# Kernel tuning notes

Measured on AMD Instinct MI355X. Metric: run time of the kernel, lower is better.

The kernel has to match this reference:

```python
import jax, jax.numpy as jnp
import numpy as np

T = 2048      # total tokens (single prefill sequence)
HID = 2048    # hidden_size
H = 16        # num k-heads == num v-heads
DK = 128      # key head dim
DV = 128      # value head dim
K = 4         # causal conv kernel width
EPS = 1e-6


def setup_inputs() -> dict:
    key = jax.random.key(0)
    ks = jax.random.split(key, 10)
    n = lambda k, shape, sc: (jax.random.normal(k, shape, jnp.float32) * sc)
    return {
        "hidden_states": n(ks[0], (T, HID), 1.0),
        "Wq": n(ks[1], (HID, H * DK), 0.02),
        "Wk": n(ks[2], (HID, H * DK), 0.02),
        "Wv": n(ks[3], (HID, H * DV), 0.02),
        "Wb": n(ks[4], (HID, H), 0.02),
        "conv_wq": n(ks[5], (H * DK, K), 0.5),
        "conv_wk": n(ks[6], (H * DK, K), 0.5),
        "conv_wv": n(ks[7], (H * DV, K), 0.5),
        "o_norm_w": jnp.ones((DV,), jnp.float32),
        "Wo": n(ks[8], (HID, HID), 0.02),
    }


def _causal_conv_silu(x, w):
    # x: [T, D], w: [D, K] depthwise causal conv, then SiLU (matches causal_conv1d_fn)
    xp = jnp.pad(x, ((K - 1, 0), (0, 0)))
    y = sum(xp[j:j + T] * w[:, j] for j in range(K))
    return jax.nn.silu(y)


def _l2norm(x):
    return x * jax.lax.rsqrt(jnp.sum(x * x, axis=-1, keepdims=True) + EPS)


def reference(hidden_states, Wq, Wk, Wv, Wb, conv_wq, conv_wk, conv_wv, o_norm_w, Wo):
    # projections [T, H*D]
    q = _causal_conv_silu(hidden_states @ Wq, conv_wq).reshape(T, H, DK)
    k = _causal_conv_silu(hidden_states @ Wk, conv_wk).reshape(T, H, DK)
    v = _causal_conv_silu(hidden_states @ Wv, conv_wv).reshape(T, H, DV)
    beta = jax.nn.sigmoid(hidden_states @ Wb)  # [T, H]

    # qk l2-norm + scale (FLA chunk_delta_rule defaults)
    q = _l2norm(q) * (DK ** -0.5)
    k = _l2norm(k)

    # delta-rule recurrence: S <- S + beta * k (v - k^T S)
    def step(S, inp):
        q_t, k_t, v_t, b_t = inp            # [H,DK],[H,DK],[H,DV],[H]
        kS = jnp.einsum('hk,hkv->hv', k_t, S)
        delta = b_t[:, None] * (v_t - kS)   # [H, DV]
        S = S + jnp.einsum('hk,hv->hkv', k_t, delta)
        o_t = jnp.einsum('hk,hkv->hv', q_t, S)
        return S, o_t

    S0 = jnp.zeros((H, DK, DV), jnp.float32)
    _, o = jax.lax.scan(step, S0, (q, k, v, beta))  # o: [T, H, DV]

    # per-head RMSNorm on value head dim
    o = o * jax.lax.rsqrt(jnp.mean(o * o, axis=-1, keepdims=True) + EPS) * o_norm_w
    out = o.reshape(T, H * DV) @ Wo
    return out
```

## Files before the change

### kernel.cpp

```cpp
#include <hip/hip_runtime.h>

typedef unsigned short u16;
typedef __attribute__((ext_vector_type(4))) unsigned short u16x4;
typedef __attribute__((ext_vector_type(8))) unsigned short u16x8;
typedef __attribute__((ext_vector_type(8))) short short8;
typedef __attribute__((ext_vector_type(4))) float f32x4;

#define DEVI __device__ __forceinline__

DEVI u16 f2b(float f) {
  union { float f; unsigned u; } x; x.f = f;
  unsigned r = (x.u + 0x7fffu + ((x.u >> 16) & 1u)) >> 16;
  return (u16)r;
}
DEVI float b2f(u16 h) {
  union { unsigned u; float f; } x; x.u = ((unsigned)h) << 16;
  return x.f;
}
DEVI f32x4 mfma_bf16(short8 a, short8 b, f32x4 c) {
  return __builtin_amdgcn_mfma_f32_16x16x32_bf16(a, b, c, 0, 0, 0);
}
DEVI void gl2lds16(const u16* g, u16* l) {
  __builtin_amdgcn_global_load_lds((__attribute__((address_space(1))) void*)g,
                                   (__attribute__((address_space(3))) void*)l,
                                   16, 0, 0);
}
DEVI void barrier_lds() {
  asm volatile("s_waitcnt lgkmcnt(0)\n\ts_barrier" ::: "memory");
}

__global__ void k_cvt(const float* __restrict__ src, u16* __restrict__ dst, int n4,
                      const float* __restrict__ Wb, u16* __restrict__ WbT) {
  int b = blockIdx.x;
  if (b < 4096) {
    int i = b * 256 + threadIdx.x;
    if (i < n4) {
      float4 v = ((const float4*)src)[i];
      u16x4 r; r.x = f2b(v.x); r.y = f2b(v.y); r.z = f2b(v.z); r.w = f2b(v.w);
      ((u16x4*)dst)[i] = r;
    }
  } else {
    int j = (b - 4096) * 256 + threadIdx.x;
    int n = j >> 11, k = j & 2047;
    WbT[j] = f2b(Wb[k * 16 + n]);
  }
}

__global__ __launch_bounds__(256)
void k_transpose4(const float* __restrict__ s0, const float* __restrict__ s1,
                  const float* __restrict__ s2, const float* __restrict__ s3,
                  u16* __restrict__ d0, u16* __restrict__ d1,
                  u16* __restrict__ d2, u16* __restrict__ d3) {
  const int RC = 2048;
  const float* src = (blockIdx.z == 0) ? s0 : (blockIdx.z == 1) ? s1 : (blockIdx.z == 2) ? s2 : s3;
  u16* dst = (blockIdx.z == 0) ? d0 : (blockIdx.z == 1) ? d1 : (blockIdx.z == 2) ? d2 : d3;
  __shared__ u16 tile[64 * 66];
  int bx = blockIdx.x << 6, by = blockIdx.y << 6;
  int x = threadIdx.x & 63, g = threadIdx.x >> 6;
#pragma unroll
  for (int i = 0; i < 16; ++i) {
    int r = (i << 2) + g;
    tile[x * 66 + r] = f2b(src[(size_t)(by + r) * RC + bx + x]);
  }
  __syncthreads();
#pragma unroll
  for (int i = 0; i < 16; ++i) {
    int r = (i << 2) + g;
    dst[(size_t)(bx + r) * RC + by + x] = tile[r * 66 + x];
  }
}

__global__ __launch_bounds__(256, 4)
void k_gemm_bt(const u16* __restrict__ A, const u16* __restrict__ BT,
               float* __restrict__ Cf, u16* __restrict__ Cb,
               int M, int N, int K, int outbf) {
  __shared__ __align__(16) u16 As[4096];
  __shared__ __align__(16) u16 Bs[4096];
  const int tid = threadIdx.x, wave = tid >> 6, lane = tid & 63;
  const long bm = (long)blockIdx.y << 7, bn = (long)blockIdx.x << 7;
  const int r0 = (wave << 4) + (lane >> 2);
  const int kof = (((lane & 3) ^ ((lane >> 3) & 3)) << 3);
  const u16* gA = A + (bm + r0) * (long)K + kof;
  const u16* gB = BT + (bn + r0) * (long)K + kof;
  u16* lA = As + (wave << 9);
  u16* lB = Bs + (wave << 9);
  const long stepR = (long)64 * K;
  const int wr = (wave >> 1) << 6, wc = (wave & 1) << 6;
  const int fr = lane & 15, fq = (lane >> 4) << 3;
  const int fqs = fq ^ (((fr >> 1) & 3) << 3);
  f32x4 acc[4][4];
#pragma unroll
  for (int i = 0; i < 4; ++i)
#pragma unroll
    for (int j = 0; j < 4; ++j) acc[i][j] = (f32x4){0.f, 0.f, 0.f, 0.f};
  for (int k0 = 0; k0 < K; k0 += 32) {
    gl2lds16(gA + k0, lA);
    gl2lds16(gA + stepR + k0, lA + 2048);
    gl2lds16(gB + k0, lB);
    gl2lds16(gB + stepR + k0, lB + 2048);
    __syncthreads();
    short8 af[4], bfr[4];
#pragma unroll
    for (int t = 0; t < 4; ++t)
      af[t] = *(const short8*)&As[(wr + (t << 4) + fr) * 32 + fqs];
#pragma unroll
    for (int t = 0; t < 4; ++t)
      bfr[t] = *(const short8*)&Bs[(wc + (t << 4) + fr) * 32 + fqs];
#pragma unroll
    for (int i = 0; i < 4; ++i)
#pragma unroll
      for (int j = 0; j < 4; ++j)
        acc[i][j] = mfma_bf16(af[i], bfr[j], acc[i][j]);
    __syncthreads();
  }
  const int er = (lane >> 4) << 2, ec = lane & 15;
#pragma unroll
  for (int i = 0; i < 4; ++i)
#pragma unroll
    for (int j = 0; j < 4; ++j)
#pragma unroll
      for (int r = 0; r < 4; ++r) {
        long row = bm + wr + (i << 4) + er + r;
        long col = bn + wc + (j << 4) + ec;
        if (outbf) Cb[row * N + col] = f2b(acc[i][j][r]);
        else       Cf[row * N + col] = acc[i][j][r];
      }
}

__global__ __launch_bounds__(256, 4)
void k_gemm_wo(const u16* __restrict__ A, const u16* __restrict__ BT,
               float* __restrict__ Cf, int M, int N, int K) {
  __shared__ __align__(16) u16 As[2048];
  __shared__ __align__(16) u16 Bs[2048];
  const int tid = threadIdx.x, wave = tid >> 6, lane = tid & 63;
  const long bm = (long)blockIdx.y << 6, bn = (long)blockIdx.x << 6;
  const int r0 = (wave << 4) + (lane >> 2);
  const int kof = (((lane & 3) ^ ((lane >> 3) & 3)) << 3);
  const u16* gA = A + (bm + r0) * (long)K + kof;
  const u16* gB = BT + (bn + r0) * (long)K + kof;
  u16* lA = As + (wave << 9);
  u16* lB = Bs + (wave << 9);
  const int wr = (wave >> 1) << 5, wc = (wave & 1) << 5;
  const int fr = lane & 15, fq = (lane >> 4) << 3;
  const int fqs = fq ^ (((fr >> 1) & 3) << 3);
  f32x4 acc[2][2];
#pragma unroll
  for (int i = 0; i < 2; ++i)
#pragma unroll
    for (int j = 0; j < 2; ++j) acc[i][j] = (f32x4){0.f, 0.f, 0.f, 0.f};
  for (int k0 = 0; k0 < K; k0 += 32) {
    gl2lds16(gA + k0, lA);
    gl2lds16(gB + k0, lB);
    __syncthreads();
    short8 af[2], bfr[2];
#pragma unroll
    for (int t = 0; t < 2; ++t) {
      af[t]  = *(const short8*)&As[(wr + (t << 4) + fr) * 32 + fqs];
      bfr[t] = *(const short8*)&Bs[(wc + (t << 4) + fr) * 32 + fqs];
    }
#pragma unroll
    for (int i = 0; i < 2; ++i)
#pragma unroll
      for (int j = 0; j < 2; ++j)
        acc[i][j] = mfma_bf16(af[i], bfr[j], acc[i][j]);
    __syncthreads();
  }
  const int er = (lane >> 4) << 2, ec = lane & 15;
#pragma unroll
  for (int i = 0; i < 2; ++i)
#pragma unroll
    for (int j = 0; j < 2; ++j)
#pragma unroll
      for (int r = 0; r < 4; ++r) {
        long row = bm + wr + (i << 4) + er + r;
        long col = bn + wc + (j << 4) + ec;
        Cf[row * N + col] = acc[i][j][r];
      }
}

__global__ __launch_bounds__(256, 4)
void k_beta(const u16* __restrict__ Xb, const u16* __restrict__ WbT,
            float* __restrict__ beta) {
  __shared__ float part[4][256];
  int tid = threadIdx.x, w = tid >> 6, lane = tid & 63;
  int t0 = blockIdx.x << 4;
  int fr = lane & 15, fq = (lane >> 4) << 3;
  const u16* ap = Xb + (size_t)(t0 + fr) * 2048 + (w << 9) + fq;
  const u16* bp = WbT + (size_t)fr * 2048 + (w << 9) + fq;
  f32x4 acc = {0.f, 0.f, 0.f, 0.f};
#pragma unroll
  for (int ks = 0; ks < 16; ++ks)
    acc = mfma_bf16(*(const short8*)(ap + (ks << 5)), *(const short8*)(bp + (ks << 5)), acc);
  int er = (lane >> 4) << 2;
#pragma unroll
  for (int r = 0; r < 4; ++r) part[w][(er + r) * 16 + fr] = acc[r];
  __syncthreads();
  float s = part[0][tid] + part[1][tid] + part[2][tid] + part[3][tid];
  beta[(t0 << 4) + tid] = 1.f / (1.f + __expf(-s));
}

__global__ __launch_bounds__(256, 4)
void k_conv(const u16* __restrict__ qkv,
            const float* __restrict__ cwq, const float* __restrict__ cwk,
            const float* __restrict__ cwv,
            u16* __restrict__ qn, u16* __restrict__ kn, u16* __restrict__ vn) {
  __shared__ __align__(16) u16 xs[67 * 136];
  __shared__ float wf[128 * 4];
  int tt = blockIdx.x, s = blockIdx.y;
  int kind = s >> 4, h = s & 15;
  int t0 = tt << 6;
  int col = (kind << 11) + (h << 7);
  int tid = threadIdx.x;
  const float* cw = (kind == 0) ? cwq : ((kind == 1) ? cwk : cwv);
  if (tid < 128) *(float4*)&wf[tid << 2] = *(const float4*)(cw + (size_t)((h << 7) + tid) * 4);
  for (int i = tid; i < 1072; i += 256) {
    int prow = i >> 4, c8 = (i & 15) << 3;
    int g = t0 - 3 + prow;
    u16x8 v = {0, 0, 0, 0, 0, 0, 0, 0};
    if (g >= 0) v = *(const u16x8*)(qkv + (size_t)g * 6144 + col + c8);
    *(u16x8*)&xs[prow * 136 + c8] = v;
  }
  __syncthreads();
  int t = tid >> 2, dg = tid & 3;
  float y[32];
  float ss = 0.f;
#pragma unroll
  for (int e8 = 0; e8 < 4; ++e8) {
    int d0 = (dg << 5) + (e8 << 3);
    u16x8 a0 = *(const u16x8*)&xs[(t + 0) * 136 + d0];
    u16x8 a1 = *(const u16x8*)&xs[(t + 1) * 136 + d0];
    u16x8 a2 = *(const u16x8*)&xs[(t + 2) * 136 + d0];
    u16x8 a3 = *(const u16x8*)&xs[(t + 3) * 136 + d0];
#pragma unroll
    for (int e = 0; e < 8; ++e) {
      float4 w = *(const float4*)&wf[(d0 + e) << 2];
      float v = b2f(a0[e]) * w.x + b2f(a1[e]) * w.y + b2f(a2[e]) * w.z + b2f(a3[e]) * w.w;
      v = v / (1.f + __expf(-v));
      y[(e8 << 3) + e] = v;
      ss += v * v;
    }
  }
  float sc = 1.f;
  if (kind < 2) {
    ss += __shfl_xor(ss, 1);
    ss += __shfl_xor(ss, 2);
    sc = rsqrtf(ss + 1e-6f);
    if (kind == 0) sc *= 0.08838834764831843f;
  }
  u16* dst = (kind == 0) ? qn : ((kind == 1) ? kn : vn);
  u16* dp = dst + ((size_t)h << 18) + ((size_t)(t0 + t) << 7) + (dg << 5);
#pragma unroll
  for (int e8 = 0; e8 < 4; ++e8) {
    u16x8 p;
#pragma unroll
    for (int e = 0; e < 8; ++e) p[e] = f2b(y[(e8 << 3) + e] * sc);
    *(u16x8*)(dp + (e8 << 3)) = p;
  }
}

__global__ __launch_bounds__(256, 2)
void k_prep(const u16* __restrict__ qn, const u16* __restrict__ kn, const u16* __restrict__ vn,
            const float* __restrict__ beta,
            u16* __restrict__ Gg, u16* __restrict__ Wg,
            u16* __restrict__ KTg, u16* __restrict__ UTg) {
  __shared__ __align__(16) char sm[70912];
  u16*  Kc  = (u16*)sm;
  u16*  Qc  = (u16*)(sm + 17408);
  u16*  Vc  = (u16*)(sm + 34816);
  u16*  KTl = (u16*)(sm + 52224);
  float* AL = (float*)(sm + 52224);
  float* Bl = (float*)(sm + 70656);
  u16*  WR  = Qc;
  int h = blockIdx.x, c = blockIdx.y;
  int tid = threadIdx.x, wave = tid >> 6, lane = tid & 63;
  size_t ch = (size_t)(c * 16 + h);
  const u16* kb = kn + ((size_t)h << 18) + ((size_t)c << 13);
  const u16* qb = qn + ((size_t)h << 18) + ((size_t)c << 13);
  const u16* vb = vn + ((size_t)h << 18) + ((size_t)c << 13);
#pragma unroll
  for (int s = 0; s < 4; ++s) {
    int e = (tid + (s << 8)) << 3;
    int t = e >> 7, d = e & 127;
    *(u16x8*)&Kc[t * 136 + d] = *(const u16x8*)(kb + e);
    *(u16x8*)&Qc[t * 136 + d] = *(const u16x8*)(qb + e);
    *(u16x8*)&Vc[t * 136 + d] = *(const u16x8*)(vb + e);
  }
  if (tid < 64) Bl[tid] = beta[((c << 6) + tid) * 16 + h];
  __syncthreads();
  int fr = lane & 15, fq = (lane >> 4) << 3, q4 = (lane >> 4) << 2;
  int arow = (wave << 4) + fr;
  f32x4 kk[4], qk[4];
#pragma unroll
  for (int ct = 0; ct < 4; ++ct) { kk[ct] = (f32x4){0.f,0.f,0.f,0.f}; qk[ct] = (f32x4){0.f,0.f,0.f,0.f}; }
#pragma unroll
  for (int ks = 0; ks < 4; ++ks) {
    short8 aK = *(const short8*)&Kc[arow * 136 + (ks << 5) + fq];
    short8 aQ = *(const short8*)&Qc[arow * 136 + (ks << 5) + fq];
#pragma unroll
    for (int ct = 0; ct < 4; ++ct) {
      short8 bK = *(const short8*)&Kc[((ct << 4) + fr) * 136 + (ks << 5) + fq];
      kk[ct] = mfma_bf16(aK, bK, kk[ct]);
      qk[ct] = mfma_bf16(aQ, bK, qk[ct]);
    }
  }
#pragma unroll
  for (int ct = 0; ct < 4; ++ct)
#pragma unroll
    for (int r = 0; r < 4; ++r) {
      int i = (wave << 4) + q4 + r, j = (ct << 4) + fr;
      Gg[(ch << 12) + i * 64 + j] = f2b((j <= i) ? qk[ct][r] : 0.f);
    }
  {
    int d = tid & 127, tg = tid >> 7;
#pragma unroll
    for (int it = 0; it < 4; ++it) {
      int t0 = (tg + (it << 1)) << 3;
      u16x8 pk;
#pragma unroll
      for (int j = 0; j < 8; ++j) pk[j] = Kc[(t0 + j) * 136 + d];
      *(u16x8*)&KTl[d * 72 + t0] = pk;
    }
  }
  __syncthreads();
#pragma unroll
  for (int it = 0; it < 4; ++it) {
    int idx = tid + (it << 8);
    int row = idx >> 3, j8 = (idx & 7) << 3;
    *(u16x8*)(KTg + (ch << 13) + (row << 6) + j8) = *(const u16x8*)&KTl[row * 72 + j8];
  }
  __syncthreads();
  {
    float bi[4];
#pragma unroll
    for (int r = 0; r < 4; ++r) bi[r] = Bl[(wave << 4) + q4 + r];
#pragma unroll
    for (int ct = 0; ct < 4; ++ct)
#pragma unroll
      for (int r = 0; r < 4; ++r) {
        int i = (wave << 4) + q4 + r, j = (ct << 4) + fr;
        AL[i * 64 + j] = (j < i) ? bi[r] * kk[ct][r] : 0.f;
      }
  }
  __syncthreads();
  float X[64];
  {
    const u16* colp = (tid < 128) ? (Kc + tid) : (Vc + (tid - 128));
#pragma unroll
    for (int t = 0; t < 64; ++t) X[t] = Bl[t] * b2f(colp[t * 136]);
#pragma unroll
    for (int r = 1; r < 64; ++r) {
      float s = 0.f;
      const float* Ar = &AL[r * 64];
      int r4 = r & ~3;
#pragma unroll
      for (int l = 0; l < 64; l += 4)
        if (l + 4 <= r) {
          float4 a = *(const float4*)(Ar + l);
          s += a.x * X[l] + a.y * X[l + 1] + a.z * X[l + 2] + a.w * X[l + 3];
        }
#pragma unroll
      for (int l = 0; l < 4; ++l)
        if (r4 + l < r) s += Ar[r4 + l] * X[r4 + l];
      X[r] -= s;
    }
  }
  __syncthreads();
  if (tid < 128) {
#pragma unroll
    for (int t = 0; t < 64; ++t) WR[t * 136 + tid] = f2b(X[t]);
  } else {
    int v = tid - 128;
    u16* dstr = UTg + (ch << 13) + (v << 6);
#pragma unroll
    for (int j = 0; j < 8; ++j) {
      u16x8 p;
#pragma unroll
      for (int e = 0; e < 8; ++e) p[e] = f2b(X[(j << 3) + e]);
      *(u16x8*)(dstr + (j << 3)) = p;
    }
  }
  __syncthreads();
#pragma unroll
  for (int it = 0; it < 4; ++it) {
    int idx = tid + (it << 8);
    int row = idx >> 4, j8 = (idx & 15) << 3;
    *(u16x8*)(Wg + (ch << 13) + (row << 7) + j8) = *(const u16x8*)&WR[row * 136 + j8];
  }
}

struct Frags { short8 q[4], w[4], g[2], k[4]; u16x4 u; };

DEVI void load_frags(Frags& f, const u16* qh, const u16* Wg, const u16* Gg,
                     const u16* KTg, const u16* UTg, int c, int h,
                     int trow, int fr, int fq, int q4, int w, int vbase) {
  const u16* qb = qh + ((size_t)((c << 6) + trow + fr) << 7) + fq;
#pragma unroll
  for (int ks = 0; ks < 4; ++ks) f.q[ks] = *(const short8*)(qb + (ks << 5));
  size_t ch = (size_t)(c * 16 + h);
  const u16* wb = Wg + (ch << 13) + ((size_t)(trow + fr) << 7) + fq;
#pragma unroll
  for (int ks = 0; ks < 4; ++ks) f.w[ks] = *(const short8*)(wb + (ks << 5));
  const u16* gb = Gg + (ch << 12) + ((size_t)(trow + fr) << 6) + fq;
#pragma unroll
  for (int ks = 0; ks < 2; ++ks) f.g[ks] = *(const short8*)(gb + (ks << 5));
  const u16* kbp = KTg + (ch << 13) + ((size_t)(w << 5) << 6) + fq;
#pragma unroll
  for (int dt = 0; dt < 2; ++dt)
#pragma unroll
    for (int ks = 0; ks < 2; ++ks)
      f.k[(dt << 1) | ks] = *(const short8*)(kbp + ((size_t)((dt << 4) + fr) << 6) + (ks << 5));
  f.u = *(const u16x4*)(UTg + (ch << 13) + ((size_t)(vbase + fr) << 6) + trow + q4);
}

DEVI void chunk_body(int c, Frags& f, u16* ST, u16* DT, u16* oh,
                     int trow, int fr, int fq, int q4, int w, int vbase,
                     f32x4& S0, f32x4& S1) {
#pragma unroll
  for (int r = 0; r < 4; ++r) {
    ST[(q4 + r) * 136 + (w << 5) + fr] = f2b(S0[r]);
    ST[(q4 + r) * 136 + (w << 5) + 16 + fr] = f2b(S1[r]);
  }
  barrier_lds();
  short8 sf[4];
#pragma unroll
  for (int ks = 0; ks < 4; ++ks) sf[ks] = *(const short8*)&ST[fr * 136 + (ks << 5) + fq];
  f32x4 racc = {0.f,0.f,0.f,0.f}, oacc = {0.f,0.f,0.f,0.f};
#pragma unroll
  for (int ks = 0; ks < 4; ++ks) {
    racc = mfma_bf16(f.w[ks], sf[ks], racc);
    oacc = mfma_bf16(f.q[ks], sf[ks], oacc);
  }
#pragma unroll
  for (int r = 0; r < 4; ++r)
    DT[fr * 72 + trow + q4 + r] = f2b(b2f(f.u[r]) - racc[r]);
  barrier_lds();
  short8 df[2];
#pragma unroll
  for (int ks = 0; ks < 2; ++ks) df[ks] = *(const short8*)&DT[fr * 72 + (ks << 5) + fq];
#pragma unroll
  for (int ks = 0; ks < 2; ++ks) {
    oacc = mfma_bf16(f.g[ks], df[ks], oacc);
    S0 = mfma_bf16(df[ks], f.k[ks], S0);
    S1 = mfma_bf16(df[ks], f.k[2 | ks], S1);
  }
#pragma unroll
  for (int r = 0; r < 4; ++r)
    oh[(size_t)((c << 6) + trow + q4 + r) * 128 + vbase + fr] = f2b(oacc[r]);
}

__global__ __launch_bounds__(256, 1)
void k_delta(const u16* __restrict__ qn, const u16* __restrict__ Wg,
             const u16* __restrict__ Gg, const u16* __restrict__ KTg,
             const u16* __restrict__ UTg, u16* __restrict__ o) {
  __shared__ __align__(16) u16 ST[16 * 136];
  __shared__ __align__(16) u16 DT[16 * 72];
  int bx = blockIdx.x;
  int h = bx & 15, vbase = (bx >> 4) << 4;
  int tid = threadIdx.x, w = tid >> 6, lane = tid & 63;
  int fr = lane & 15, fq = (lane >> 4) << 3, q4 = (lane >> 4) << 2;
  int trow = w << 4;
  const u16* qh = qn + ((size_t)h << 18);
  u16* oh = o + ((size_t)h << 18);
  f32x4 S0 = {0.f,0.f,0.f,0.f}, S1 = {0.f,0.f,0.f,0.f};
  Frags fa, fb;
  load_frags(fa, qh, Wg, Gg, KTg, UTg, 0, h, trow, fr, fq, q4, w, vbase);
  for (int c = 0; c < 32; c += 2) {
    int c1 = c + 1, c2 = (c + 2 < 32) ? c + 2 : 31;
    load_frags(fb, qh, Wg, Gg, KTg, UTg, c1, h, trow, fr, fq, q4, w, vbase);
    chunk_body(c, fa, ST, DT, oh, trow, fr, fq, q4, w, vbase, S0, S1);
    load_frags(fa, qh, Wg, Gg, KTg, UTg, c2, h, trow, fr, fq, q4, w, vbase);
    chunk_body(c1, fb, ST, DT, oh, trow, fr, fq, q4, w, vbase, S0, S1);
  }
}

__global__ __launch_bounds__(256, 4)
void k_onorm(const u16* __restrict__ o, const float* __restrict__ onw,
             u16* __restrict__ onb) {
  __shared__ float wl[128];
  int tt = blockIdx.x, h = blockIdx.y, tid = threadIdx.x;
  if (tid < 128) wl[tid] = onw[tid];
  __syncthreads();
  int t = tid >> 2, dg = tid & 3;
  const u16* src = o + ((size_t)h << 18) + ((size_t)((tt << 6) + t) << 7) + (dg << 5);
  u16x8 a[4];
  float ss = 0.f;
#pragma unroll
  for (int e8 = 0; e8 < 4; ++e8) {
    a[e8] = *(const u16x8*)(src + (e8 << 3));
#pragma unroll
    for (int e = 0; e < 8; ++e) { float x = b2f(a[e8][e]); ss += x * x; }
  }
  ss += __shfl_xor(ss, 1);
  ss += __shfl_xor(ss, 2);
  float inv = rsqrtf(ss * (1.f / 128.f) + 1e-6f);
  u16* dp = onb + ((size_t)((tt << 6) + t) << 11) + (h << 7) + (dg << 5);
#pragma unroll
  for (int e8 = 0; e8 < 4; ++e8) {
    u16x8 p;
#pragma unroll
    for (int e = 0; e < 8; ++e)
      p[e] = f2b(b2f(a[e8][e]) * inv * wl[(dg << 5) + (e8 << 3) + e]);
    *(u16x8*)(dp + (e8 << 3)) = p;
  }
}

extern "C" void kernel_launch(void* const* d_in, const int* in_sizes, int n_in,
                              void* d_out, int out_size, void* d_ws, size_t ws_size,
                              hipStream_t stream) {
  (void)in_sizes; (void)n_in; (void)out_size; (void)ws_size;
  const float* hs  = (const float*)d_in[0];
  const float* Wq  = (const float*)d_in[1];
  const float* Wk  = (const float*)d_in[2];
  const float* Wv  = (const float*)d_in[3];
  const float* Wb  = (const float*)d_in[4];
  const float* cwq = (const float*)d_in[5];
  const float* cwk = (const float*)d_in[6];
  const float* cwv = (const float*)d_in[7];
  const float* onw = (const float*)d_in[8];
  const float* Wo  = (const float*)d_in[9];
  float* out = (float*)d_out;
  char* ws = (char*)d_ws;
  const size_t MB = 1ull << 20;
  u16*  Xb   = (u16*)(ws);
  u16*  WT   = (u16*)(ws + 8  * MB);
  u16*  WoT  = (u16*)(ws + 32 * MB);
  u16*  QKV  = (u16*)(ws + 40 * MB);
  u16*  Wg   = (u16*)(ws + 40 * MB);
  u16*  KTg  = (u16*)(ws + 48 * MB);
  u16*  UTg  = (u16*)(ws + 56 * MB);
  u16*  qn_  = (u16*)(ws + 64 * MB);
  u16*  kn_  = (u16*)(ws + 72 * MB);
  u16*  vn_  = (u16*)(ws + 80 * MB);
  float* beta= (float*)(ws + 88 * MB);
  u16*  WbT  = (u16*)(ws + 88 * MB + 512 * 1024);
  u16*  Gm   = (u16*)(ws + 89 * MB);
  u16*  o_   = (u16*)(ws + 93 * MB);
  u16*  onb  = (u16*)(ws + 109 * MB);

  k_cvt<<<4224, 256, 0, stream>>>(hs, Xb, 2048 * 2048 / 4, Wb, WbT);
  k_transpose4<<<dim3(32, 32, 4), 256, 0, stream>>>(
      Wq, Wk, Wv, Wo, WT, WT + 2048 * 2048, WT + 2 * 2048 * 2048, WoT);
  k_gemm_bt<<<dim3(48, 16), 256, 0, stream>>>(Xb, WT, nullptr, QKV, 2048, 6144, 2048, 1);
  k_beta<<<128, 256, 0, stream>>>(Xb, WbT, beta);
  k_conv<<<dim3(32, 48), 256, 0, stream>>>(QKV, cwq, cwk, cwv, qn_, kn_, vn_);
  k_prep<<<dim3(16, 32), 256, 0, stream>>>(qn_, kn_, vn_, beta, Gm, Wg, KTg, UTg);
  k_delta<<<128, 256, 0, stream>>>(qn_, Wg, Gm, KTg, UTg, o_);
  k_onorm<<<dim3(32, 16), 256, 0, stream>>>(o_, onw, onb);
  k_gemm_wo<<<dim3(32, 32), 256, 0, stream>>>(onb, WoT, out, 2048, 2048, 2048);
}
```

Baseline: 345.4 us.

## Replace QKV GEMM with 256x256 tiled, double-buffered 8-wave pipelined kernel

Replaces the 128x128 single-buffered QKV projection GEMM with a 256x256-tile, 512-thread kernel that uses a 128 KB double-buffered LDS pipeline. Global-to-LDS loads for the next K-tile are issued in quarter-tile stages between MFMA phases, using explicit barriers, waitcnt and setprio. The intent is to raise data reuse per block and hide load latency behind tensor-core work. In exchange the grid shrinks to 192 blocks, which may underfill the CUs, and the hand-scheduled waits and swizzles add correctness risk.

```diff
diff --git a/kernel.cpp b/kernel.cpp
--- a/kernel.cpp
+++ b/kernel.cpp
@@ -70,61 +70,170 @@
   }
 }
 
-__global__ __launch_bounds__(256, 4)
-void k_gemm_bt(const u16* __restrict__ A, const u16* __restrict__ BT,
-               float* __restrict__ Cf, u16* __restrict__ Cb,
-               int M, int N, int K, int outbf) {
-  __shared__ __align__(16) u16 As[4096];
-  __shared__ __align__(16) u16 Bs[4096];
+
+struct StageCtx { size_t go[2]; int lo[2]; };
+
+DEVI void stage_half(const u16* g, const StageCtx& sc, u16* l) {
+  gl2lds16(g + sc.go[0], l + sc.lo[0]);
+  gl2lds16(g + sc.go[1], l + sc.lo[1]);
+}
+
+template <int MODE>
+DEVI void ktile8(const u16* gA0, const u16* gA1, const u16* gB0, const u16* gB1,
+                 const StageCtx& sc, u16* lds, int u,
+                 const int (&aoff)[4][2], const int (&boff)[2][2],
+                 f32x4 (&acc)[8][4]) {
+  const int sl = (u & 1) << 13, sl1 = ((u + 1) & 1) << 13;
+  const u16* hA0 = lds + sl;
+  const u16* hA1 = lds + 16384 + sl;
+  const u16* hB0 = lds + 32768 + sl;
+  const u16* hB1 = lds + 49152 + sl;
+  const size_t uo1 = (size_t)(u + 1) << 6, uo2 = (size_t)(u + 2) << 6;
+  short8 a[4][2], b0[2][2], b1[2][2];
+#pragma unroll
+  for (int m = 0; m < 4; ++m) {
+    a[m][0] = *(const short8*)(hA0 + aoff[m][0]);
+    a[m][1] = *(const short8*)(hA0 + aoff[m][1]);
+  }
+#pragma unroll
+  for (int n = 0; n < 2; ++n) {
+    b0[n][0] = *(const short8*)(hB0 + boff[n][0]);
+    b0[n][1] = *(const short8*)(hB0 + boff[n][1]);
+  }
+  if constexpr (MODE <= 1) stage_half(gA1 + uo1, sc, lds + 16384 + sl1);
+  __builtin_amdgcn_s_barrier();
+  asm volatile("s_waitcnt lgkmcnt(0)" ::: "memory");
+  __builtin_amdgcn_s_setprio(1);
+#pragma unroll
+  for (int m = 0; m < 4; ++m)
+#pragma unroll
+    for (int n = 0; n < 2; ++n) {
+      acc[m][n] = mfma_bf16(a[m][0], b0[n][0], acc[m][n]);
+      acc[m][n] = mfma_bf16(a[m][1], b0[n][1], acc[m][n]);
+    }
+  __builtin_amdgcn_s_setprio(0);
+  __builtin_amdgcn_s_barrier();
+#pragma unroll
+  for (int n = 0; n < 2; ++n) {
+    b1[n][0] = *(const short8*)(hB1 + boff[n][0]);
+    b1[n][1] = *(const short8*)(hB1 + boff[n][1]);
+  }
+  if constexpr (MODE == 0) stage_half(gA0 + uo2, sc, lds + sl);
+  __builtin_amdgcn_s_barrier();
+  asm volatile("s_waitcnt lgkmcnt(0)" ::: "memory");
+  __builtin_amdgcn_s_setprio(1);
+#pragma unroll
+  for (int m = 0; m < 4; ++m)
+#pragma unroll
+    for (int n = 0; n < 2; ++n) {
+      acc[m][2 + n] = mfma_bf16(a[m][0], b1[n][0], acc[m][2 + n]);
+      acc[m][2 + n] = mfma_bf16(a[m][1], b1[n][1], acc[m][2 + n]);
+    }
+  __builtin_amdgcn_s_setprio(0);
+  __builtin_amdgcn_s_barrier();
+#pragma unroll
+  for (int m = 0; m < 4; ++m) {
+    a[m][0] = *(const short8*)(hA1 + aoff[m][0]);
+    a[m][1] = *(const short8*)(hA1 + aoff[m][1]);
+  }
+  if constexpr (MODE == 0) stage_half(gB0 + uo2, sc, lds + 32768 + sl);
+  __builtin_amdgcn_s_barrier();
+  asm volatile("s_waitcnt lgkmcnt(0)" ::: "memory");
+  __builtin_amdgcn_s_setprio(1);
+#pragma unroll
+  for (int m = 0; m < 4; ++m)
+#pragma unroll
+    for (int n = 0; n < 2; ++n) {
+      acc[4 + m][n] = mfma_bf16(a[m][0], b0[n][0], acc[4 + m][n]);
+      acc[4 + m][n] = mfma_bf16(a[m][1], b0[n][1], acc[4 + m][n]);
+    }
+  __builtin_amdgcn_s_setprio(0);
+  __builtin_amdgcn_s_barrier();
+  if constexpr (MODE == 0) stage_half(gB1 + uo2, sc, lds + 49152 + sl);
+  __builtin_amdgcn_s_barrier();
+  __builtin_amdgcn_s_setprio(1);
+#pragma unroll
+  for (int m = 0; m < 4; ++m)
+#pragma unroll
+    for (int n = 0; n < 2; ++n) {
+      acc[4 + m][2 + n] = mfma_bf16(a[m][0], b1[n][0], acc[4 + m][2 + n]);
+      acc[4 + m][2 + n] = mfma_bf16(a[m][1], b1[n][1], acc[4 + m][2 + n]);
+    }
+  __builtin_amdgcn_s_setprio(0);
+  if constexpr (MODE == 0) asm volatile("s_waitcnt vmcnt(6)" ::: "memory");
+  if constexpr (MODE == 1) asm volatile("s_waitcnt vmcnt(0)" ::: "memory");
+  __builtin_amdgcn_s_barrier();
+}
+
+__global__ __launch_bounds__(512, 2)
+void k_gemm8p(const u16* __restrict__ A, const u16* __restrict__ BT,
+              u16* __restrict__ Cb, int N, int K) {
+  __shared__ __align__(16) u16 lds[65536];
   const int tid = threadIdx.x, wave = tid >> 6, lane = tid & 63;
-  const long bm = (long)blockIdx.y << 7, bn = (long)blockIdx.x << 7;
-  const int r0 = (wave << 4) + (lane >> 2);
-  const int kof = (((lane & 3) ^ ((lane >> 3) & 3)) << 3);
-  const u16* gA = A + (bm + r0) * (long)K + kof;
-  const u16* gB = BT + (bn + r0) * (long)K + kof;
-  u16* lA = As + (wave << 9);
-  u16* lB = Bs + (wave << 9);
-  const long stepR = (long)64 * K;
-  const int wr = (wave >> 1) << 6, wc = (wave & 1) << 6;
-  const int fr = lane & 15, fq = (lane >> 4) << 3;
-  const int fqs = fq ^ (((fr >> 1) & 3) << 3);
-  f32x4 acc[4][4];
-#pragma unroll
-  for (int i = 0; i < 4; ++i)
+  const int wm = wave >> 2, wn = wave & 3;
+  const int fr = lane & 15, fq = (lane >> 4) << 4;
+  const long bm = (long)blockIdx.y << 8, bn = (long)blockIdx.x << 8;
+  const int NT = K >> 6;
+  int aoff[4][2], boff[2][2];
+#pragma unroll
+  for (int m = 0; m < 4; ++m)
+#pragma unroll
+    for (int ks = 0; ks < 2; ++ks) {
+      int row = (wm << 6) + (m << 4) + fr;
+      int kb = (ks << 6) + fq;
+      aoff[m][ks] = (row << 6) + ((kb ^ ((fr & 7) << 4)) >> 1);
+    }
+#pragma unroll
+  for (int n = 0; n < 2; ++n)
+#pragma unroll
+    for (int ks = 0; ks < 2; ++ks) {
+      int row = (wn << 5) + (n << 4) + fr;
+      int kb = (ks << 6) + fq;
+      boff[n][ks] = (row << 6) + ((kb ^ ((fr & 7) << 4)) >> 1);
+    }
+  StageCtx sc;
+#pragma unroll
+  for (int s = 0; s < 2; ++s) {
+    int c = (s << 9) + tid, row = c >> 3;
+    int kbs = (((c & 7) << 4) ^ ((row & 7) << 4));
+    sc.go[s] = (size_t)row * K + (kbs >> 1);
+    sc.lo[s] = ((s << 9) + (tid & ~63)) << 3;
+  }
+  const u16* gA0 = A + (size_t)bm * K;
+  const u16* gA1 = gA0 + (size_t)128 * K;
+  const u16* gB0 = BT + (size_t)bn * K;
+  const u16* gB1 = gB0 + (size_t)128 * K;
+  f32x4 acc[8][4];
+#pragma unroll
+  for (int i = 0; i < 8; ++i)
 #pragma unroll
     for (int j = 0; j < 4; ++j) acc[i][j] = (f32x4){0.f, 0.f, 0.f, 0.f};
-  for (int k0 = 0; k0 < K; k0 += 32) {
-    gl2lds16(gA + k0, lA);
-    gl2lds16(gA + stepR + k0, lA + 2048);
-    gl2lds16(gB + k0, lB);
-    gl2lds16(gB + stepR + k0, lB + 2048);
-    __syncthreads();
-    short8 af[4], bfr[4];
-#pragma unroll
-    for (int t = 0; t < 4; ++t)
-      af[t] = *(const short8*)&As[(wr + (t << 4) + fr) * 32 + fqs];
-#pragma unroll
-    for (int t = 0; t < 4; ++t)
-      bfr[t] = *(const short8*)&Bs[(wc + (t << 4) + fr) * 32 + fqs];
-#pragma unroll
-    for (int i = 0; i < 4; ++i)
-#pragma unroll
-      for (int j = 0; j < 4; ++j)
-        acc[i][j] = mfma_bf16(af[i], bfr[j], acc[i][j]);
-    __syncthreads();
-  }
+  stage_half(gA0, sc, lds + 0);
+  stage_half(gA1, sc, lds + 16384);
+  stage_half(gB0, sc, lds + 32768);
+  stage_half(gB1, sc, lds + 49152);
+  asm volatile("s_waitcnt vmcnt(4)" ::: "memory");
+  stage_half(gA0 + 64, sc, lds + 8192);
+  stage_half(gB0 + 64, sc, lds + 40960);
+  stage_half(gB1 + 64, sc, lds + 57344);
+  asm volatile("s_waitcnt vmcnt(6)" ::: "memory");
+  __builtin_amdgcn_s_barrier();
+  for (int u = 0; u + 2 < NT; ++u)
+    ktile8<0>(gA0, gA1, gB0, gB1, sc, lds, u, aoff, boff, acc);
+  ktile8<1>(gA0, gA1, gB0, gB1, sc, lds, NT - 2, aoff, boff, acc);
+  ktile8<2>(gA0, gA1, gB0, gB1, sc, lds, NT - 1, aoff, boff, acc);
   const int er = (lane >> 4) << 2, ec = lane & 15;
 #pragma unroll
-  for (int i = 0; i < 4; ++i)
-#pragma unroll
-    for (int j = 0; j < 4; ++j)
-#pragma unroll
-      for (int r = 0; r < 4; ++r) {
-        long row = bm + wr + (i << 4) + er + r;
-        long col = bn + wc + (j << 4) + ec;
-        if (outbf) Cb[row * N + col] = f2b(acc[i][j][r]);
-        else       Cf[row * N + col] = acc[i][j][r];
-      }
+  for (int ai = 0; ai < 8; ++ai) {
+    long row0 = bm + ((long)(ai >> 2) << 7) + (wm << 6) + ((ai & 3) << 4) + er;
+#pragma unroll
+    for (int bj = 0; bj < 4; ++bj) {
+      long col = bn + ((long)(bj >> 1) << 7) + (wn << 5) + ((bj & 1) << 4) + ec;
+#pragma unroll
+      for (int r = 0; r < 4; ++r)
+        Cb[(size_t)(row0 + r) * N + col] = f2b(acc[ai][bj][r]);
+    }
+  }
 }
 
 __global__ __launch_bounds__(256, 4)
@@ -540,7 +649,7 @@
   k_cvt<<<4224, 256, 0, stream>>>(hs, Xb, 2048 * 2048 / 4, Wb, WbT);
   k_transpose4<<<dim3(32, 32, 4), 256, 0, stream>>>(
       Wq, Wk, Wv, Wo, WT, WT + 2048 * 2048, WT + 2 * 2048 * 2048, WoT);
-  k_gemm_bt<<<dim3(48, 16), 256, 0, stream>>>(Xb, WT, nullptr, QKV, 2048, 6144, 2048, 1);
+  k_gemm8p<<<dim3(24, 8), 512, 0, stream>>>(Xb, WT, QKV, 6144, 2048);
   k_beta<<<128, 256, 0, stream>>>(Xb, WbT, beta);
   k_conv<<<dim3(32, 48), 256, 0, stream>>>(QKV, cwq, cwk, cwv, qn_, kn_, vn_);
   k_prep<<<dim3(16, 32), 256, 0, stream>>>(qn_, kn_, vn_, beta, Gm, Wg, KTg, UTg);
```

Result: no change. 340.7 us (-1.4%).
